# Kernel tuning notes

Measured on AMD Instinct MI355X. Metric: run time of the kernel, lower is better.

## Reference

```python
import jax, jax.numpy as jnp
import numpy as np

B, N, M = 32, 512, 32          # batch frames, atoms, neighbors
H_A = 64                        # atom embedding dim
DMIN, DMAX, STEP = 0.0, 10.0, 0.1
FILTERS = jnp.arange(DMIN, DMAX + STEP, STEP, dtype=jnp.float32)  # [101]
H_B = FILTERS.shape[0]
N_CONV = 4
N_CLASSES = 10
BN_EPS = 1e-5


def setup_inputs() -> dict:
    key = jax.random.key(0)
    ks = jax.random.split(key, 6)
    return {
        "nbr_adj_dist": jax.random.uniform(ks[0], (B, N, M), jnp.float32) * DMAX,
        "nbr_adj_list": jax.random.randint(ks[1], (B, N, M), 0, N),
        "emb_w": jax.random.normal(ks[2], (N, H_A), jnp.float32),
        "fc_w": jax.random.normal(ks[3], (N_CONV, 2 * H_A + H_B, 2 * H_A), jnp.float32) * 0.05,
        "fc_b": jnp.zeros((N_CONV, 2 * H_A), jnp.float32),
        "bn1_g": jnp.ones((N_CONV, 2 * H_A), jnp.float32),
        "bn1_b": jnp.zeros((N_CONV, 2 * H_A), jnp.float32),
        "bn2_g": jnp.ones((N_CONV, H_A), jnp.float32),
        "bn2_b": jnp.zeros((N_CONV, H_A), jnp.float32),
        "cls_w": jax.random.normal(ks[4], (H_A, N_CLASSES), jnp.float32) * 0.05,
        "cls_b": jnp.zeros((N_CLASSES,), jnp.float32),
    }


def _bn(x2d, g, b):
    # training-mode BatchNorm1d over flattened batch axis (biased variance)
    mu = x2d.mean(axis=0)
    var = x2d.var(axis=0)
    return g * (x2d - mu) * jax.lax.rsqrt(var + BN_EPS) + b


def reference(nbr_adj_dist, nbr_adj_list, emb_w, fc_w, fc_b,
              bn1_g, bn1_b, bn2_g, bn2_b, cls_w, cls_b):
    # 1. Gaussian basis expansion of neighbor distances: [B,N,M,H_B]
    nbr_emb = jnp.exp(-((nbr_adj_dist[..., None] - FILTERS) ** 2) / (STEP ** 2))
    # 2. atom embeddings: atom_emb_idx = arange(N) per batch element
    atom = jnp.broadcast_to(emb_w[None], (B, N, H_A))
    # 3. CGCNN-style graph convolutions
    for l in range(N_CONV):
        # neighbor gather per batch: [B,N,M,H_A]
        nbrs = jax.vmap(lambda e, idx: e[idx])(atom, nbr_adj_list)
        total = jnp.concatenate(
            [jnp.broadcast_to(atom[:, :, None, :], (B, N, M, H_A)), nbrs, nbr_emb],
            axis=-1)                                        # [B,N,M,2*H_A+H_B]
        gated = jnp.einsum('bnmf,fh->bnmh', total, fc_w[l]) + fc_b[l]
        gated = _bn(gated.reshape(-1, 2 * H_A), bn1_g[l], bn1_b[l]).reshape(B, N, M, 2 * H_A)
        filt, core = jnp.split(gated, 2, axis=-1)
        summed = jnp.sum(jax.nn.sigmoid(filt) * jax.nn.relu(core), axis=2)  # [B,N,H_A]
        summed = _bn(summed.reshape(-1, H_A), bn2_g[l], bn2_b[l]).reshape(B, N, H_A)
        atom = jax.nn.relu(atom + summed)  # layer-internal residual
    # 4-6. activation, mean pooling over atoms, classifier, softmax
    emb = jax.nn.relu(atom)
    pooled = jnp.sum(emb, axis=1) / N                      # [B,H_A]
    logits = pooled @ cls_w + cls_b                        # [B,n_classes]
    return jax.nn.softmax(logits, axis=-1)
```

## Files before the change

### kernel.cpp

```cpp
#include <hip/hip_runtime.h>
#include <math.h>

typedef _Float16 half_t;
typedef __attribute__((ext_vector_type(4))) _Float16 half4;

constexpr int kB   = 32;
constexpr int kN   = 512;
constexpr int kM   = 32;
constexpr int kHA  = 64;
constexpr int kHB  = 101;
constexpr int kHO  = 128;
constexpr int kNF  = 229;
constexpr int kRows = kB * kN;
constexpr long kTRows = (long)kRows * kM;
constexpr int kNCls = 10;
constexpr float kEps = 1e-5f;
constexpr int kG    = 8;
constexpr int kNB   = kRows / kG;
constexpr int kT    = 512;
constexpr int kS    = 4096;

__device__ __forceinline__ int origCh(int j) {
    return ((j & 1) << 6) + ((j >> 2) << 1) + ((j >> 1) & 1);
}

__global__ void k_init_atom(const float* __restrict__ emb, float* __restrict__ atom) {
    int i = blockIdx.x * blockDim.x + threadIdx.x;
    atom[i] = emb[i & (kN * kHA - 1)];
}

template<bool RESID>
__global__ __launch_bounds__(256)
void k_pre(const float* __restrict__ atomIn, float* __restrict__ atomOut,
           const float* __restrict__ summed, const float* __restrict__ acc2,
           const float* __restrict__ g2, const float* __restrict__ b2,
           const float* __restrict__ W, const float* __restrict__ bias,
           float* __restrict__ preA, float* __restrict__ preB,
           float* __restrict__ bn1acc, float* __restrict__ zeroBuf) {
    __shared__ float sA[32 * 64];
    __shared__ float sc2s[128];
    int t = threadIdx.x;
    if (blockIdx.x == 0) {
        bn1acc[t] = 0.f;
        if (t < 128) zeroBuf[t] = 0.f;
    }
    if (RESID) {
        if (t < 64) {
            float inv = 1.f / (float)kRows;
            float mu = acc2[t] * inv;
            float var = acc2[64 + t] * inv - mu * mu;
            float sc = g2[t] * rsqrtf(var + kEps);
            sc2s[t] = sc;
            sc2s[64 + t] = b2[t] - mu * sc;
        }
        __syncthreads();
    }
    int r0 = blockIdx.x * 32;
    for (int i = t; i < 32 * 64; i += 256) {
        float v = atomIn[r0 * 64 + i];
        if (RESID) {
            int h = i & 63;
            v = fmaxf(v + fmaf(summed[r0 * 64 + i], sc2s[h], sc2s[64 + h]), 0.f);
            atomOut[r0 * 64 + i] = v;
        }
        sA[i] = v;
    }
    __syncthreads();
    int cg = t & 31, rg = t >> 5;
    float2 bb01 = *(const float2*)&bias[2 * cg];
    float2 bb23 = *(const float2*)&bias[64 + 2 * cg];
    float4 accA[4], accB[4];
    #pragma unroll
    for (int r = 0; r < 4; ++r) {
        accA[r] = make_float4(bb01.x, bb23.x, bb01.y, bb23.y);
        accB[r] = make_float4(0.f, 0.f, 0.f, 0.f);
    }
    for (int k = 0; k < 64; ++k) {
        float2 wA01 = *(const float2*)&W[k * kHO + 2 * cg];
        float2 wA23 = *(const float2*)&W[k * kHO + 64 + 2 * cg];
        float2 wB01 = *(const float2*)&W[(64 + k) * kHO + 2 * cg];
        float2 wB23 = *(const float2*)&W[(64 + k) * kHO + 64 + 2 * cg];
        #pragma unroll
        for (int r = 0; r < 4; ++r) {
            float a = sA[(rg * 4 + r) * 64 + k];
            accA[r].x = fmaf(a, wA01.x, accA[r].x);
            accA[r].y = fmaf(a, wA23.x, accA[r].y);
            accA[r].z = fmaf(a, wA01.y, accA[r].z);
            accA[r].w = fmaf(a, wA23.y, accA[r].w);
            accB[r].x = fmaf(a, wB01.x, accB[r].x);
            accB[r].y = fmaf(a, wB23.x, accB[r].y);
            accB[r].z = fmaf(a, wB01.y, accB[r].z);
            accB[r].w = fmaf(a, wB23.y, accB[r].w);
        }
    }
    #pragma unroll
    for (int r = 0; r < 4; ++r) {
        int row = r0 + rg * 4 + r;
        *(float4*)&preA[row * kHO + 4 * cg] = accA[r];
        *(float4*)&preB[row * kHO + 4 * cg] = accB[r];
    }
}

__global__ __launch_bounds__(128)
void k_table(const float* __restrict__ W3, half_t* __restrict__ tab) {
    __shared__ float wv[13];
    int s = blockIdx.x;
    int t = threadIdx.x;
    float d = (float)s * (10.f / (float)kS);
    int kc = (int)floorf(d * 10.f);
    int ks = min(max(kc - 6, 0), kHB - 13);
    if (t < 13) {
        float dd = d - 0.1f * (float)(ks + t);
        wv[t] = __expf(-100.f * dd * dd);
    }
    __syncthreads();
    int oc = origCh(t);
    float a = 0.f;
    #pragma unroll
    for (int j = 0; j < 13; ++j)
        a = fmaf(wv[j], W3[(ks + j) * kHO + oc], a);
    tab[s * kHO + t] = (half_t)a;
}

__global__ __launch_bounds__(kT, 6)
void k_stats(const float* __restrict__ dist, const int* __restrict__ nbrs,
             const float* __restrict__ preA, const float* __restrict__ preB,
             const half_t* __restrict__ tab, float* __restrict__ acc) {
    __shared__ int   roff[kG][kM];
    __shared__ int   soff[kG][kM];
    __shared__ float sfrac[kG][kM];
    __shared__ float red[2048];
    int t = threadIdx.x;
    int lb = (int)(blockIdx.x & 7) * (kNB / 8) + (int)(blockIdx.x >> 3);
    if (t < kG * kM) {
        int g = t >> 5, m = t & 31;
        int p = lb * kG + g;
        float d = dist[p * kM + m];
        float sf = d * ((float)kS / 10.f);
        int s = min((int)sf, kS - 1);
        soff[g][m] = s * kHO;
        sfrac[g][m] = sf - (float)s;
        roff[g][m] = (((p >> 9) << 9) + nbrs[p * kM + m]) * kHO;
    }
    __syncthreads();
    int cg = t & 31, ms = t >> 5;
    float S[4] = {0.f, 0.f, 0.f, 0.f}, SS[4] = {0.f, 0.f, 0.f, 0.f};
    for (int g = 0; g < kG; ++g) {
        int p = lb * kG + g;
        float4 pa = *(const float4*)&preA[p * kHO + 4 * cg];
        #pragma unroll
        for (int mm = 0; mm < 2; ++mm) {
            int m = ms + mm * 16;
            int ro = roff[g][m], so = soff[g][m];
            float fr = sfrac[g][m];
            float4 pb = *(const float4*)&preB[ro + 4 * cg];
            half4 lo = *(const half4*)&tab[so + 4 * cg];
            half4 hi = *(const half4*)&tab[so + kHO + 4 * cg];
            float l0 = (float)lo.x, l1 = (float)lo.y, l2 = (float)lo.z, l3 = (float)lo.w;
            float t0 = fmaf(fr, (float)hi.x - l0, l0);
            float t1 = fmaf(fr, (float)hi.y - l1, l1);
            float t2 = fmaf(fr, (float)hi.z - l2, l2);
            float t3 = fmaf(fr, (float)hi.w - l3, l3);
            float x0 = pa.x + pb.x + t0, x1 = pa.y + pb.y + t1;
            float x2 = pa.z + pb.z + t2, x3 = pa.w + pb.w + t3;
            S[0] += x0; S[1] += x1; S[2] += x2; S[3] += x3;
            SS[0] = fmaf(x0, x0, SS[0]); SS[1] = fmaf(x1, x1, SS[1]);
            SS[2] = fmaf(x2, x2, SS[2]); SS[3] = fmaf(x3, x3, SS[3]);
        }
    }
    #pragma unroll
    for (int c = 0; c < 4; ++c) {
        S[c]  += __shfl_xor(S[c], 32);
        SS[c] += __shfl_xor(SS[c], 32);
    }
    int w = t >> 6;
    if ((t & 63) < 32) {
        *(float4*)&red[w * 128 + cg * 4] = make_float4(S[0], S[1], S[2], S[3]);
        *(float4*)&red[1024 + w * 128 + cg * 4] = make_float4(SS[0], SS[1], SS[2], SS[3]);
    }
    __syncthreads();
    if (t < 256) {
        int j = t & 127, sel = t >> 7;
        float s = 0.f;
        #pragma unroll
        for (int ww = 0; ww < 8; ++ww) s += red[sel * 1024 + ww * 128 + j];
        atomicAdd(&acc[sel * 128 + j], s);
    }
}

__global__ __launch_bounds__(kT, 6)
void k_apply(const float* __restrict__ dist, const int* __restrict__ nbrs,
             const float* __restrict__ preA, const float* __restrict__ preB,
             const half_t* __restrict__ tab, const float* __restrict__ acc,
             const float* __restrict__ g1, const float* __restrict__ b1,
             float* __restrict__ summed, float* __restrict__ acc2) {
    __shared__ int   roff[kG][kM];
    __shared__ int   soff[kG][kM];
    __shared__ float sfrac[kG][kM];
    __shared__ float scP[128], shP[128];
    __shared__ float red2[512];
    int t = threadIdx.x;
    int lb = (int)(blockIdx.x & 7) * (kNB / 8) + (int)(blockIdx.x >> 3);
    if (t < kG * kM) {
        int g = t >> 5, m = t & 31;
        int p = lb * kG + g;
        float d = dist[p * kM + m];
        float sf = d * ((float)kS / 10.f);
        int s = min((int)sf, kS - 1);
        soff[g][m] = s * kHO;
        sfrac[g][m] = sf - (float)s;
        roff[g][m] = (((p >> 9) << 9) + nbrs[p * kM + m]) * kHO;
    }
    if (t < 128) {
        float inv = 1.f / (float)kTRows;
        int oc = origCh(t);
        float mu = acc[t] * inv;
        float var = acc[128 + t] * inv - mu * mu;
        float sc = g1[oc] * rsqrtf(var + kEps);
        scP[t] = sc;
        shP[t] = b1[oc] - mu * sc;
    }
    __syncthreads();
    int cg = t & 31, ms = t >> 5;
    float4 sc4 = *(const float4*)&scP[4 * cg];
    float4 sh4 = *(const float4*)&shP[4 * cg];
    float S2 = 0.f, SS2 = 0.f;
    for (int g = 0; g < kG; ++g) {
        int p = lb * kG + g;
        float4 pa = *(const float4*)&preA[(size_t)p * kHO + 4 * cg];
        float s0 = 0.f, s1 = 0.f;
        #pragma unroll
        for (int mm = 0; mm < 2; ++mm) {
            int m = ms + mm * 16;
            int ro = roff[g][m], so = soff[g][m];
            float fr = sfrac[g][m];
            float4 pb = *(const float4*)&preB[(size_t)ro + 4 * cg];
            half4 lo = *(const half4*)&tab[so + 4 * cg];
            half4 hi = *(const half4*)&tab[so + kHO + 4 * cg];
            float l0 = (float)lo.x, l1 = (float)lo.y, l2 = (float)lo.z, l3 = (float)lo.w;
            float t0 = fmaf(fr, (float)hi.x - l0, l0);
            float t1 = fmaf(fr, (float)hi.y - l1, l1);
            float t2 = fmaf(fr, (float)hi.z - l2, l2);
            float t3 = fmaf(fr, (float)hi.w - l3, l3);
            float x0 = pa.x + pb.x + t0, x1 = pa.y + pb.y + t1;
            float x2 = pa.z + pb.z + t2, x3 = pa.w + pb.w + t3;
            float yf0 = fmaf(x0, sc4.x, sh4.x);
            float yc0 = fmaf(x1, sc4.y, sh4.y);
            float yf1 = fmaf(x2, sc4.z, sh4.z);
            float yc1 = fmaf(x3, sc4.w, sh4.w);
            float sg0 = 1.f / (1.f + __expf(-yf0));
            float sg1 = 1.f / (1.f + __expf(-yf1));
            s0 = fmaf(sg0, fmaxf(yc0, 0.f), s0);
            s1 = fmaf(sg1, fmaxf(yc1, 0.f), s1);
        }
        s0 += __shfl_xor(s0, 32);
        s1 += __shfl_xor(s1, 32);
        int w = t >> 6;
        if ((t & 63) < 32)
            *(float2*)&red2[w * 64 + cg * 2] = make_float2(s0, s1);
        __syncthreads();
        if (t < 64) {
            float v = 0.f;
            #pragma unroll
            for (int ww = 0; ww < 8; ++ww) v += red2[ww * 64 + t];
            summed[(size_t)p * kHA + t] = v;
            S2 += v;
            SS2 = fmaf(v, v, SS2);
        }
        __syncthreads();
    }
    if (t < 64) {
        atomicAdd(&acc2[t], S2);
        atomicAdd(&acc2[64 + t], SS2);
    }
}

__global__ __launch_bounds__(1024)
void k_final(const float* __restrict__ atom, const float* __restrict__ summed,
             const float* __restrict__ acc2, const float* __restrict__ g2,
             const float* __restrict__ b2, const float* __restrict__ cw,
             const float* __restrict__ cb, float* __restrict__ out) {
    __shared__ float red[1024];
    __shared__ float sc2s[128];
    __shared__ float pooled[kHA];
    __shared__ float lg[kNCls];
    int b = blockIdx.x, t = threadIdx.x;
    if (t < 64) {
        float inv = 1.f / (float)kRows;
        float mu = acc2[t] * inv;
        float var = acc2[64 + t] * inv - mu * mu;
        float sc = g2[t] * rsqrtf(var + kEps);
        sc2s[t] = sc;
        sc2s[64 + t] = b2[t] - mu * sc;
    }
    __syncthreads();
    int h = t & 63, q = t >> 6;
    const float* ab = atom + (long)b * kN * kHA;
    const float* sb = summed + (long)b * kN * kHA;
    float scv = sc2s[h], shv = sc2s[64 + h];
    float s = 0.f;
    for (int n = q * 32; n < q * 32 + 32; ++n) {
        float v = ab[n * 64 + h] + fmaf(sb[n * 64 + h], scv, shv);
        s += fmaxf(v, 0.f);
    }
    red[t] = s;
    __syncthreads();
    if (t < 64) {
        float v = 0.f;
        #pragma unroll
        for (int qq = 0; qq < 16; ++qq) v += red[qq * 64 + t];
        pooled[t] = v * (1.f / kN);
    }
    __syncthreads();
    if (t < kNCls) {
        float a = cb[t];
        #pragma unroll
        for (int k = 0; k < kHA; ++k) a = fmaf(pooled[k], cw[k * kNCls + t], a);
        lg[t] = a;
    }
    __syncthreads();
    if (t == 0) {
        float mx = lg[0];
        for (int c = 1; c < kNCls; ++c) mx = fmaxf(mx, lg[c]);
        float e[kNCls], se = 0.f;
        for (int c = 0; c < kNCls; ++c) { e[c] = __expf(lg[c] - mx); se += e[c]; }
        float inv = 1.f / se;
        for (int c = 0; c < kNCls; ++c) out[b * kNCls + c] = e[c] * inv;
    }
}

extern "C" void kernel_launch(void* const* d_in, const int* in_sizes, int n_in,
                              void* d_out, int out_size, void* d_ws, size_t ws_size,
                              hipStream_t stream) {
    const float* dist = (const float*)d_in[0];
    const int*   nbrs = (const int*)d_in[1];
    const float* emb  = (const float*)d_in[2];
    const float* fcw  = (const float*)d_in[3];
    const float* fcb  = (const float*)d_in[4];
    const float* bn1g = (const float*)d_in[5];
    const float* bn1b = (const float*)d_in[6];
    const float* bn2g = (const float*)d_in[7];
    const float* bn2b = (const float*)d_in[8];
    const float* clw  = (const float*)d_in[9];
    const float* clb  = (const float*)d_in[10];
    float* out = (float*)d_out;

    float* ws     = (float*)d_ws;
    float* atom   = ws;
    float* preA   = atom + kRows * kHA;
    float* preB   = preA + kRows * kHO;
    float* summed = preB + kRows * kHO;
    float* bn1acc = summed + kRows * kHA;
    float* acc2a  = bn1acc + 256;
    float* acc2b  = acc2a + 128;
    half_t* tab   = (half_t*)(acc2b + 128);

    k_init_atom<<<dim3(kRows * kHA / 256), dim3(256), 0, stream>>>(emb, atom);
    for (int l = 0; l < 4; ++l) {
        const float* W  = fcw + (long)l * kNF * kHO;
        const float* W3 = W + 2 * kHA * kHO;
        float* accW = (l & 1) ? acc2b : acc2a;
        float* accR = ((l - 1) & 1) ? acc2b : acc2a;
        if (l == 0)
            k_pre<false><<<dim3(kRows / 32), dim3(256), 0, stream>>>(
                atom, atom, nullptr, nullptr, nullptr, nullptr,
                W, fcb + l * kHO, preA, preB, bn1acc, accW);
        else
            k_pre<true><<<dim3(kRows / 32), dim3(256), 0, stream>>>(
                atom, atom, summed, accR, bn2g + (l - 1) * kHA, bn2b + (l - 1) * kHA,
                W, fcb + l * kHO, preA, preB, bn1acc, accW);
        k_table<<<dim3(kS + 1), dim3(128), 0, stream>>>(W3, tab);
        k_stats<<<dim3(kNB), dim3(kT), 0, stream>>>(dist, nbrs, preA, preB, tab, bn1acc);
        k_apply<<<dim3(kNB), dim3(kT), 0, stream>>>(dist, nbrs, preA, preB, tab, bn1acc,
                                                    bn1g + l * kHO, bn1b + l * kHO,
                                                    summed, accW);
    }
    k_final<<<dim3(kB), dim3(1024), 0, stream>>>(atom, summed, acc2b,
                                                 bn2g + 3 * kHA, bn2b + 3 * kHA,
                                                 clw, clb, out);
}
```

Before: 758.8 us.

## Interleave lookup table lo/hi entries and halve block size in stats/apply

The table is rebuilt so each 8-half chunk holds entry s and entry s+1 for four channels. One 16-byte load then replaces two 8-byte loads per neighbor for the interpolation. Blocks shrink from 8 atoms/512 threads to 4 atoms/256 threads, with four neighbors per thread and a higher occupancy hint. The interleaved table doubles its memory footprint, and there are twice as many blocks, each issuing its own atomics.

```diff
diff --git a/kernel.cpp b/kernel.cpp
--- a/kernel.cpp
+++ b/kernel.cpp
@@ -2,7 +2,7 @@
 #include <math.h>
 
 typedef _Float16 half_t;
-typedef __attribute__((ext_vector_type(4))) _Float16 half4;
+typedef __attribute__((ext_vector_type(8))) _Float16 half8;
 
 constexpr int kB   = 32;
 constexpr int kN   = 512;
@@ -15,9 +15,9 @@
 constexpr long kTRows = (long)kRows * kM;
 constexpr int kNCls = 10;
 constexpr float kEps = 1e-5f;
-constexpr int kG    = 8;
+constexpr int kG    = 4;
 constexpr int kNB   = kRows / kG;
-constexpr int kT    = 512;
+constexpr int kT    = 256;
 constexpr int kS    = 4096;
 
 __device__ __forceinline__ int origCh(int j) {
@@ -102,7 +102,7 @@
 }
 
 __global__ __launch_bounds__(128)
-void k_table(const float* __restrict__ W3, half_t* __restrict__ tab) {
+void k_table(const float* __restrict__ W3, half_t* __restrict__ tabQ) {
     __shared__ float wv[13];
     int s = blockIdx.x;
     int t = threadIdx.x;
@@ -119,17 +119,20 @@
     #pragma unroll
     for (int j = 0; j < 13; ++j)
         a = fmaf(wv[j], W3[(ks + j) * kHO + oc], a);
-    tab[s * kHO + t] = (half_t)a;
-}
-
-__global__ __launch_bounds__(kT, 6)
+    half_t h = (half_t)a;
+    int cq = t >> 2, e = t & 3;
+    if (s < kS) tabQ[s * 256 + cq * 8 + e] = h;
+    if (s > 0)  tabQ[(s - 1) * 256 + cq * 8 + 4 + e] = h;
+}
+
+__global__ __launch_bounds__(kT, 8)
 void k_stats(const float* __restrict__ dist, const int* __restrict__ nbrs,
              const float* __restrict__ preA, const float* __restrict__ preB,
-             const half_t* __restrict__ tab, float* __restrict__ acc) {
+             const half_t* __restrict__ tabQ, float* __restrict__ acc) {
     __shared__ int   roff[kG][kM];
     __shared__ int   soff[kG][kM];
     __shared__ float sfrac[kG][kM];
-    __shared__ float red[2048];
+    __shared__ float red[1024];
     int t = threadIdx.x;
     int lb = (int)(blockIdx.x & 7) * (kNB / 8) + (int)(blockIdx.x >> 3);
     if (t < kG * kM) {
@@ -138,7 +141,7 @@
         float d = dist[p * kM + m];
         float sf = d * ((float)kS / 10.f);
         int s = min((int)sf, kS - 1);
-        soff[g][m] = s * kHO;
+        soff[g][m] = s * 256;
         sfrac[g][m] = sf - (float)s;
         roff[g][m] = (((p >> 9) << 9) + nbrs[p * kM + m]) * kHO;
     }
@@ -147,20 +150,20 @@
     float S[4] = {0.f, 0.f, 0.f, 0.f}, SS[4] = {0.f, 0.f, 0.f, 0.f};
     for (int g = 0; g < kG; ++g) {
         int p = lb * kG + g;
-        float4 pa = *(const float4*)&preA[p * kHO + 4 * cg];
-        #pragma unroll
-        for (int mm = 0; mm < 2; ++mm) {
-            int m = ms + mm * 16;
+        float4 pa = *(const float4*)&preA[(size_t)p * kHO + 4 * cg];
+        #pragma unroll
+        for (int mm = 0; mm < 4; ++mm) {
+            int m = ms + mm * 8;
             int ro = roff[g][m], so = soff[g][m];
             float fr = sfrac[g][m];
-            float4 pb = *(const float4*)&preB[ro + 4 * cg];
-            half4 lo = *(const half4*)&tab[so + 4 * cg];
-            half4 hi = *(const half4*)&tab[so + kHO + 4 * cg];
-            float l0 = (float)lo.x, l1 = (float)lo.y, l2 = (float)lo.z, l3 = (float)lo.w;
-            float t0 = fmaf(fr, (float)hi.x - l0, l0);
-            float t1 = fmaf(fr, (float)hi.y - l1, l1);
-            float t2 = fmaf(fr, (float)hi.z - l2, l2);
-            float t3 = fmaf(fr, (float)hi.w - l3, l3);
+            float4 pb = *(const float4*)&preB[(size_t)ro + 4 * cg];
+            half8 tv = *(const half8*)&tabQ[so + cg * 8];
+            float l0 = (float)tv.s0, l1 = (float)tv.s1;
+            float l2 = (float)tv.s2, l3 = (float)tv.s3;
+            float t0 = fmaf(fr, (float)tv.s4 - l0, l0);
+            float t1 = fmaf(fr, (float)tv.s5 - l1, l1);
+            float t2 = fmaf(fr, (float)tv.s6 - l2, l2);
+            float t3 = fmaf(fr, (float)tv.s7 - l3, l3);
             float x0 = pa.x + pb.x + t0, x1 = pa.y + pb.y + t1;
             float x2 = pa.z + pb.z + t2, x3 = pa.w + pb.w + t3;
             S[0] += x0; S[1] += x1; S[2] += x2; S[3] += x3;
@@ -176,29 +179,29 @@
     int w = t >> 6;
     if ((t & 63) < 32) {
         *(float4*)&red[w * 128 + cg * 4] = make_float4(S[0], S[1], S[2], S[3]);
-        *(float4*)&red[1024 + w * 128 + cg * 4] = make_float4(SS[0], SS[1], SS[2], SS[3]);
-    }
-    __syncthreads();
-    if (t < 256) {
+        *(float4*)&red[512 + w * 128 + cg * 4] = make_float4(SS[0], SS[1], SS[2], SS[3]);
+    }
+    __syncthreads();
+    {
         int j = t & 127, sel = t >> 7;
         float s = 0.f;
         #pragma unroll
-        for (int ww = 0; ww < 8; ++ww) s += red[sel * 1024 + ww * 128 + j];
+        for (int ww = 0; ww < 4; ++ww) s += red[sel * 512 + ww * 128 + j];
         atomicAdd(&acc[sel * 128 + j], s);
     }
 }
 
-__global__ __launch_bounds__(kT, 6)
+__global__ __launch_bounds__(kT, 8)
 void k_apply(const float* __restrict__ dist, const int* __restrict__ nbrs,
              const float* __restrict__ preA, const float* __restrict__ preB,
-             const half_t* __restrict__ tab, const float* __restrict__ acc,
+             const half_t* __restrict__ tabQ, const float* __restrict__ acc,
              const float* __restrict__ g1, const float* __restrict__ b1,
              float* __restrict__ summed, float* __restrict__ acc2) {
     __shared__ int   roff[kG][kM];
     __shared__ int   soff[kG][kM];
     __shared__ float sfrac[kG][kM];
     __shared__ float scP[128], shP[128];
-    __shared__ float red2[512];
+    __shared__ float red2[256];
     int t = threadIdx.x;
     int lb = (int)(blockIdx.x & 7) * (kNB / 8) + (int)(blockIdx.x >> 3);
     if (t < kG * kM) {
@@ -207,7 +210,7 @@
         float d = dist[p * kM + m];
         float sf = d * ((float)kS / 10.f);
         int s = min((int)sf, kS - 1);
-        soff[g][m] = s * kHO;
+        soff[g][m] = s * 256;
         sfrac[g][m] = sf - (float)s;
         roff[g][m] = (((p >> 9) << 9) + nbrs[p * kM + m]) * kHO;
     }
@@ -230,18 +233,18 @@
         float4 pa = *(const float4*)&preA[(size_t)p * kHO + 4 * cg];
         float s0 = 0.f, s1 = 0.f;
         #pragma unroll
-        for (int mm = 0; mm < 2; ++mm) {
-            int m = ms + mm * 16;
+        for (int mm = 0; mm < 4; ++mm) {
+            int m = ms + mm * 8;
             int ro = roff[g][m], so = soff[g][m];
             float fr = sfrac[g][m];
             float4 pb = *(const float4*)&preB[(size_t)ro + 4 * cg];
-            half4 lo = *(const half4*)&tab[so + 4 * cg];
-            half4 hi = *(const half4*)&tab[so + kHO + 4 * cg];
-            float l0 = (float)lo.x, l1 = (float)lo.y, l2 = (float)lo.z, l3 = (float)lo.w;
-            float t0 = fmaf(fr, (float)hi.x - l0, l0);
-            float t1 = fmaf(fr, (float)hi.y - l1, l1);
-            float t2 = fmaf(fr, (float)hi.z - l2, l2);
-            float t3 = fmaf(fr, (float)hi.w - l3, l3);
+            half8 tv = *(const half8*)&tabQ[so + cg * 8];
+            float l0 = (float)tv.s0, l1 = (float)tv.s1;
+            float l2 = (float)tv.s2, l3 = (float)tv.s3;
+            float t0 = fmaf(fr, (float)tv.s4 - l0, l0);
+            float t1 = fmaf(fr, (float)tv.s5 - l1, l1);
+            float t2 = fmaf(fr, (float)tv.s6 - l2, l2);
+            float t3 = fmaf(fr, (float)tv.s7 - l3, l3);
             float x0 = pa.x + pb.x + t0, x1 = pa.y + pb.y + t1;
             float x2 = pa.z + pb.z + t2, x3 = pa.w + pb.w + t3;
             float yf0 = fmaf(x0, sc4.x, sh4.x);
@@ -260,9 +263,7 @@
             *(float2*)&red2[w * 64 + cg * 2] = make_float2(s0, s1);
         __syncthreads();
         if (t < 64) {
-            float v = 0.f;
-            #pragma unroll
-            for (int ww = 0; ww < 8; ++ww) v += red2[ww * 64 + t];
+            float v = red2[t] + red2[64 + t] + red2[128 + t] + red2[192 + t];
             summed[(size_t)p * kHA + t] = v;
             S2 += v;
             SS2 = fmaf(v, v, SS2);
@@ -353,7 +354,7 @@
     float* bn1acc = summed + kRows * kHA;
     float* acc2a  = bn1acc + 256;
     float* acc2b  = acc2a + 128;
-    half_t* tab   = (half_t*)(acc2b + 128);
+    half_t* tabQ  = (half_t*)(acc2b + 128);
 
     k_init_atom<<<dim3(kRows * kHA / 256), dim3(256), 0, stream>>>(emb, atom);
     for (int l = 0; l < 4; ++l) {
@@ -369,9 +370,9 @@
             k_pre<true><<<dim3(kRows / 32), dim3(256), 0, stream>>>(
                 atom, atom, summed, accR, bn2g + (l - 1) * kHA, bn2b + (l - 1) * kHA,
                 W, fcb + l * kHO, preA, preB, bn1acc, accW);
-        k_table<<<dim3(kS + 1), dim3(128), 0, stream>>>(W3, tab);
-        k_stats<<<dim3(kNB), dim3(kT), 0, stream>>>(dist, nbrs, preA, preB, tab, bn1acc);
-        k_apply<<<dim3(kNB), dim3(kT), 0, stream>>>(dist, nbrs, preA, preB, tab, bn1acc,
+        k_table<<<dim3(kS + 1), dim3(128), 0, stream>>>(W3, tabQ);
+        k_stats<<<dim3(kNB), dim3(kT), 0, stream>>>(dist, nbrs, preA, preB, tabQ, bn1acc);
+        k_apply<<<dim3(kNB), dim3(kT), 0, stream>>>(dist, nbrs, preA, preB, tabQ, bn1acc,
                                                     bn1g + l * kHO, bn1b + l * kHO,
                                                     summed, accW);
     }
```

After: 1.356 ms. 78.7% more time.
